# Kernel tuning notes

Measured on AMD Instinct MI355X. Metric: run time of the kernel, lower is better.

The kernel has to match this reference:

```python
import jax, jax.numpy as jnp
import numpy as np

B, D, N = 2048, 512, 100000


def setup_inputs() -> dict:
    key = jax.random.key(0)
    k1, k2, k3 = jax.random.split(key, 3)
    queries = jax.random.normal(k1, (B, D), dtype=jnp.float32)
    X = jax.random.normal(k2, (N, D), dtype=jnp.float32)
    Y = jax.random.randint(k3, (N,), 0, 2, dtype=jnp.int64)
    return {"queries": queries, "X": X, "Y": Y, "K": 5}


def reference(queries, X, Y, K):
    # Pairwise squared Euclidean distance: ||q||^2 - 2 q.X^T + ||x||^2.
    # Use negative distance so lax.top_k returns nearest neighbors.
    q2 = jnp.sum(queries * queries, axis=1, keepdims=True)        # [B, 1]
    x2 = jnp.sum(X * X, axis=1)                                   # [N]
    neg_dist = 2.0 * (queries @ X.T) - q2 - x2[None, :]           # [B, N]
    _, idx = jax.lax.top_k(neg_dist, K)                           # [B, K]
    # Gather neighbor labels and count votes (fraction of class-1 neighbors).
    neighbor_labels = Y[idx].astype(jnp.float32)                  # [B, K]
    votes = jnp.mean(neighbor_labels, axis=1)                     # [B]
    # tf.pad(tf.expand_dims(votes, 1), [[0,0],[0,1]]) -> [B, 2]
    return jnp.pad(votes[:, None], ((0, 0), (0, 1)))
```

## Files before the change

### kernel.cpp

```cpp
#include <hip/hip_runtime.h>
#include <math.h>

typedef unsigned int   u32;
typedef unsigned short u16;
typedef short short8 __attribute__((ext_vector_type(8)));
typedef float f32x4  __attribute__((ext_vector_type(4)));

constexpr int B    = 2048;
constexpr int D    = 512;
constexpr int N    = 100000;
constexpr int KTOP = 5;
constexpr int NK   = 16;

constexpr int NPART    = 64;
constexpr int CHUNK    = 1568;
constexpr int PGPART   = CHUNK / 16;
constexpr int NPTS_PAD = NPART * CHUNK;
constexpr int NPG      = NPTS_PAD / 16;
constexpr int ITERS    = PGPART;

__device__ __forceinline__ u16 f2bf(float f) {
    u32 u = __float_as_uint(f);
    return (u16)((u + 0x7fffu + ((u >> 16) & 1u)) >> 16);
}

__device__ __forceinline__ void gld_lds16(const void* g, void* l) {
    __builtin_amdgcn_global_load_lds((const __attribute__((address_space(1))) u32*)g,
                                     (__attribute__((address_space(3))) u32*)l, 16, 0, 0);
}

__device__ __forceinline__ void ins5(float (&s)[KTOP], int (&x)[KTOP], float v, int p) {
    if (v > s[KTOP - 1]) {
        s[KTOP - 1] = v; x[KTOP - 1] = p;
#pragma unroll
        for (int k = KTOP - 1; k > 0; --k) {
            if (s[k] > s[k - 1]) {
                float tf = s[k]; s[k] = s[k - 1]; s[k - 1] = tf;
                int   tg = x[k]; x[k] = x[k - 1]; x[k - 1] = tg;
            }
        }
    }
}

__device__ __forceinline__ void merge_xor(float (&s)[KTOP], int (&x)[KTOP], int mask) {
    float bs[KTOP], as[KTOP]; int bx[KTOP], ax[KTOP];
#pragma unroll
    for (int k = 0; k < KTOP; ++k) {
        bs[k] = __shfl_xor(s[k], mask); bx[k] = __shfl_xor(x[k], mask);
        as[k] = s[k]; ax[k] = x[k];
    }
#pragma unroll
    for (int k = 0; k < KTOP; ++k) {
        bool ta = (as[0] > bs[0]) || ((as[0] == bs[0]) && (ax[0] < bx[0]));
        s[k] = ta ? as[0] : bs[0];
        x[k] = ta ? ax[0] : bx[0];
#pragma unroll
        for (int m = 0; m < KTOP - 1; ++m) {
            as[m] = ta ? as[m + 1] : as[m];     ax[m] = ta ? ax[m + 1] : ax[m];
            bs[m] = ta ? bs[m]     : bs[m + 1]; bx[m] = ta ? bx[m]     : bx[m + 1];
        }
        as[KTOP - 1] = ta ? -INFINITY : as[KTOP - 1];
        bs[KTOP - 1] = ta ? bs[KTOP - 1] : -INFINITY;
    }
}

__global__ void prep_q(const float* __restrict__ Q, u16* __restrict__ Qbf) {
    int tid  = blockIdx.x * 256 + threadIdx.x;
    int q    = tid >> 6;
    int koct = tid & 63;
    const float4* src = (const float4*)(Q + (size_t)q * D + koct * 8);
    float4 a = src[0], b = src[1];
    u32 p0 = (u32)f2bf(a.x) | ((u32)f2bf(a.y) << 16);
    u32 p1 = (u32)f2bf(a.z) | ((u32)f2bf(a.w) << 16);
    u32 p2 = (u32)f2bf(b.x) | ((u32)f2bf(b.y) << 16);
    u32 p3 = (u32)f2bf(b.z) | ((u32)f2bf(b.w) << 16);
    int frag = (q >> 4) * NK + (koct >> 2);
    int lane = (q & 15) + 16 * (koct & 3);
    *(uint4*)(Qbf + (size_t)frag * 512 + lane * 8) = make_uint4(p0, p1, p2, p3);
}

__global__ void prep_x2(const float* __restrict__ X, u16* __restrict__ Xbf,
                        float* __restrict__ x2) {
    __shared__ float psum[4][16];
    const int t = threadIdx.x, lane = t & 63, wave = t >> 6;
    const int pg    = blockIdx.x;
    const int point = pg * 16 + (lane & 15);
    float ssum = 0.f;
#pragma unroll
    for (int u = 0; u < 4; ++u) {
        int k0i = wave * 4 + u;
        int k   = k0i * 32 + ((lane >> 4) << 3);
        uint4 o = make_uint4(0u, 0u, 0u, 0u);
        if (point < N) {
            const float4* src = (const float4*)(X + (size_t)point * D + k);
            float4 a = src[0], b = src[1];
            ssum = fmaf(a.x, a.x, ssum); ssum = fmaf(a.y, a.y, ssum);
            ssum = fmaf(a.z, a.z, ssum); ssum = fmaf(a.w, a.w, ssum);
            ssum = fmaf(b.x, b.x, ssum); ssum = fmaf(b.y, b.y, ssum);
            ssum = fmaf(b.z, b.z, ssum); ssum = fmaf(b.w, b.w, ssum);
            o.x = (u32)f2bf(a.x) | ((u32)f2bf(a.y) << 16);
            o.y = (u32)f2bf(a.z) | ((u32)f2bf(a.w) << 16);
            o.z = (u32)f2bf(b.x) | ((u32)f2bf(b.y) << 16);
            o.w = (u32)f2bf(b.z) | ((u32)f2bf(b.w) << 16);
        }
        *(uint4*)(Xbf + ((size_t)pg * 16 + k0i) * 512 + lane * 8) = o;
    }
    ssum += __shfl_xor(ssum, 16);
    ssum += __shfl_xor(ssum, 32);
    if (lane < 16) psum[wave][lane] = ssum;
    __syncthreads();
    if (t < 16) {
        float s = psum[0][t] + psum[1][t] + psum[2][t] + psum[3][t];
        x2[pg * 16 + t] = (pg * 16 + t < N) ? s : INFINITY;
    }
}

__global__ void x2_kernel(const float* __restrict__ X, float* __restrict__ x2, int total) {
    int lane = threadIdx.x & 63;
    int wid  = (int)((blockIdx.x * blockDim.x + threadIdx.x) >> 6);
    if (wid >= total) return;
    if (wid >= N) { if (lane == 0) x2[wid] = INFINITY; return; }
    const float* row = X + (size_t)wid * D;
    float s = 0.f;
    for (int c = lane; c < D; c += 64) { float v = row[c]; s = fmaf(v, v, s); }
#pragma unroll
    for (int off = 32; off > 0; off >>= 1) s += __shfl_down(s, off);
    if (lane == 0) x2[wid] = s;
}

__launch_bounds__(256, 4)
__global__ void knn_qreg(const u16* __restrict__ Xbf, const u16* __restrict__ Qbf,
                         const float* __restrict__ x2g,
                         float* __restrict__ cand_s, int* __restrict__ cand_i) {
    __shared__ __attribute__((aligned(16))) u16 Afr[2][16 * 512];
    const int t    = threadIdx.x;
    const int lane = t & 63;
    const int wave = t >> 6;
    const int quad = lane >> 4;
    const int col  = lane & 15;
    const int part = blockIdx.x;
    const int qb   = blockIdx.y;
    const int pg0    = part * PGPART;
    const int pstart = part * CHUNK;

    const int qg = qb * 4 + wave;
    short8 bq[16];
#pragma unroll
    for (int k0i = 0; k0i < 16; ++k0i)
        bq[k0i] = *(const short8*)(Qbf + ((size_t)qg * 16 + k0i) * 512 + lane * 8);
    asm volatile("" ::: "memory");

    float ss[KTOP]; int si[KTOP];
#pragma unroll
    for (int k = 0; k < KTOP; ++k) { ss[k] = -INFINITY; si[k] = 0x7fffffff; }

    auto issue = [&](int it, int bsel) {
        const size_t pgA = (size_t)(pg0 + it);
        const u16* src = Xbf + (pgA * 16 + wave * 4) * 512 + (lane << 3);
        u16* dst = Afr[bsel] + (wave * 4) * 512;
#pragma unroll
        for (int f = 0; f < 4; ++f)
            gld_lds16(src + f * 512, dst + f * 512);
    };

    issue(0, 0);
    for (int it = 0; it < ITERS; ++it) {
        const int bsel = it & 1;
        __syncthreads();
        if (it + 1 < ITERS) issue(it + 1, bsel ^ 1);
        const int PA = pstart + it * 16;
        float4 xx = *(const float4*)(x2g + PA + quad * 4);

        f32x4 acc = (f32x4)0.f;
#pragma unroll
        for (int k0i = 0; k0i < 16; ++k0i) {
            short8 af = *(const short8*)&Afr[bsel][k0i * 512 + lane * 8];
            acc = __builtin_amdgcn_mfma_f32_16x16x32_bf16(af, bq[k0i], acc, 0, 0, 0);
        }
        const int gbase = PA + quad * 4;
        float s0 = fmaf(2.f, acc[0], -xx.x);
        float s1 = fmaf(2.f, acc[1], -xx.y);
        float s2 = fmaf(2.f, acc[2], -xx.z);
        float s3 = fmaf(2.f, acc[3], -xx.w);
        float mx = fmaxf(fmaxf(s0, s1), fmaxf(s2, s3));
        if (mx > ss[KTOP - 1]) {
            ins5(ss, si, s0, gbase + 0); ins5(ss, si, s1, gbase + 1);
            ins5(ss, si, s2, gbase + 2); ins5(ss, si, s3, gbase + 3);
        }
    }

    merge_xor(ss, si, 16); merge_xor(ss, si, 32);
    if (quad == 0) {
        int q = qg * 16 + col;
        size_t base = ((size_t)q * NPART + part) * KTOP;
#pragma unroll
        for (int k = 0; k < KTOP; ++k) { cand_s[base + k] = ss[k]; cand_i[base + k] = si[k]; }
    }
}

__launch_bounds__(256)
__global__ void knn_conv(const float* __restrict__ X, const u16* __restrict__ Qbf,
                         const float* __restrict__ x2g,
                         float* __restrict__ cand_s, int* __restrict__ cand_i) {
    __shared__ __attribute__((aligned(16))) u16 Bfr[16 * 512];
    __shared__ __attribute__((aligned(16))) u16 Afr[4 * 512];
    __shared__ float x2s[64];
    const int t = threadIdx.x, lane = t & 63, wave = t >> 6;
    const int quad = lane >> 4, col = lane & 15;
    const int qb = blockIdx.x, part = blockIdx.y;
    const int pstart = part * 782;
    const int pend   = min(pstart + 782, N);

    float ss[4][KTOP]; int si[4][KTOP];
#pragma unroll
    for (int j = 0; j < 4; ++j)
#pragma unroll
        for (int k = 0; k < KTOP; ++k) { ss[j][k] = -INFINITY; si[j][k] = 0x7fffffff; }

    const int nsub = (pend - pstart + 63) / 64;
    for (int sbi = 0; sbi < nsub; ++sbi) {
        const int sb = pstart + sbi * 64;
        __syncthreads();
        if (t < 64) x2s[t] = (sb + t < pend) ? x2g[sb + t] : INFINITY;
        f32x4 acc[4][4];
#pragma unroll
        for (int i = 0; i < 4; ++i)
#pragma unroll
            for (int j = 0; j < 4; ++j) acc[i][j] = (f32x4)0.f;
        for (int k0i = 0; k0i < NK; ++k0i) {
            const int k0 = k0i * 32;
            __syncthreads();
            {
                int prow = sb + wave * 16 + col;
                if (prow >= pend) prow = pend - 1;
                const float4* src = (const float4*)(X + (size_t)prow * D + k0 + quad * 8);
                float4 a = src[0], b = src[1];
                u32 p0 = (u32)f2bf(a.x) | ((u32)f2bf(a.y) << 16);
                u32 p1 = (u32)f2bf(a.z) | ((u32)f2bf(a.w) << 16);
                u32 p2 = (u32)f2bf(b.x) | ((u32)f2bf(b.y) << 16);
                u32 p3 = (u32)f2bf(b.z) | ((u32)f2bf(b.w) << 16);
                *(uint4*)(Afr + wave * 512 + lane * 8) = make_uint4(p0, p1, p2, p3);
            }
#pragma unroll
            for (int j = 0; j < 4; ++j) {
                int qgrp = qb * 16 + wave * 4 + j;
                gld_lds16(Qbf + ((size_t)qgrp * NK + k0i) * 512 + lane * 8,
                          (void*)(Bfr + (wave * 4 + j) * 512));
            }
            __syncthreads();
            short8 af[4], bqf[4];
#pragma unroll
            for (int i = 0; i < 4; ++i) af[i] = *(const short8*)(Afr + i * 512 + lane * 8);
#pragma unroll
            for (int j = 0; j < 4; ++j) bqf[j] = *(const short8*)(Bfr + (wave * 4 + j) * 512 + lane * 8);
#pragma unroll
            for (int i = 0; i < 4; ++i)
#pragma unroll
                for (int j = 0; j < 4; ++j)
                    acc[i][j] = __builtin_amdgcn_mfma_f32_16x16x32_bf16(af[i], bqf[j], acc[i][j], 0, 0, 0);
        }
#pragma unroll
        for (int i = 0; i < 4; ++i) {
            int pb = 16 * i + quad * 4;
#pragma unroll
            for (int j = 0; j < 4; ++j)
#pragma unroll
                for (int r = 0; r < 4; ++r)
                    ins5(ss[j], si[j], 2.f * acc[i][j][r] - x2s[pb + r], sb + pb + r);
        }
    }
#pragma unroll
    for (int j = 0; j < 4; ++j) { merge_xor(ss[j], si[j], 16); merge_xor(ss[j], si[j], 32); }
    if (quad == 0) {
#pragma unroll
        for (int j = 0; j < 4; ++j) {
            int qg = qb * 256 + wave * 64 + j * 16 + col;
            size_t base = ((size_t)qg * 128 + part) * KTOP;
#pragma unroll
            for (int k = 0; k < KTOP; ++k) { cand_s[base + k] = ss[j][k]; cand_i[base + k] = si[j][k]; }
        }
    }
}

__launch_bounds__(256)
__global__ void finalize(const float* __restrict__ Q, const float* __restrict__ X,
                         const float* __restrict__ x2g, const int* __restrict__ Y,
                         const float* __restrict__ cand_s, const int* __restrict__ cand_i,
                         float* __restrict__ out, int npart) {
    __shared__ float scs[4][96];
    __shared__ int   sis[4][96];
    const int t = threadIdx.x, lane = t & 63, w = t >> 6;
    const int q = blockIdx.x * 4 + w;
    const int perlane = npart * KTOP / 16;

    if (lane < 16) {
        float ls[KTOP]; int li[KTOP];
#pragma unroll
        for (int k = 0; k < KTOP; ++k) { ls[k] = -INFINITY; li[k] = 0x7fffffff; }
        const float* cs = cand_s + (size_t)q * npart * KTOP + lane * perlane;
        const int*   ci = cand_i + (size_t)q * npart * KTOP + lane * perlane;
        for (int c = 0; c < perlane; ++c) {
            float s = cs[c]; int p = ci[c];
            if (s > ls[KTOP - 1] || (s == ls[KTOP - 1] && p < li[KTOP - 1])) {
                ls[KTOP - 1] = s; li[KTOP - 1] = p;
#pragma unroll
                for (int k = KTOP - 1; k > 0; --k) {
                    bool up = (ls[k] > ls[k - 1]) || (ls[k] == ls[k - 1] && li[k] < li[k - 1]);
                    if (up) {
                        float tf = ls[k]; ls[k] = ls[k - 1]; ls[k - 1] = tf;
                        int   tg = li[k]; li[k] = li[k - 1]; li[k - 1] = tg;
                    }
                }
            }
        }
#pragma unroll
        for (int k = 0; k < KTOP; ++k) { scs[w][lane * KTOP + k] = ls[k]; sis[w][lane * KTOP + k] = li[k]; }
    }
    __syncthreads();
    if (lane == 0) {
        float bs[16]; int bx[16];
#pragma unroll
        for (int m = 0; m < 16; ++m) { bs[m] = -INFINITY; bx[m] = 0x7fffffff; }
        for (int c = 0; c < 80; ++c) {
            float s = scs[w][c]; int p = sis[w][c];
            if (s > bs[15] || (s == bs[15] && p < bx[15])) {
                bs[15] = s; bx[15] = p;
#pragma unroll
                for (int m = 15; m > 0; --m) {
                    bool up = (bs[m] > bs[m - 1]) || (bs[m] == bs[m - 1] && bx[m] < bx[m - 1]);
                    if (up) {
                        float tf = bs[m]; bs[m] = bs[m - 1]; bs[m - 1] = tf;
                        int   tg = bx[m]; bx[m] = bx[m - 1]; bx[m - 1] = tg;
                    }
                }
            }
        }
#pragma unroll
        for (int m = 0; m < 16; ++m) sis[w][80 + m] = bx[m];
    }
    __syncthreads();
    const int c = lane & 15, seg = lane >> 4;
    int idx = sis[w][80 + c];
    const float4* xr = (const float4*)(X + (size_t)idx * D);
    const float4* qr = (const float4*)(Q + (size_t)q * D);
    float d = 0.f;
    for (int u = seg * 32; u < seg * 32 + 32; ++u) {
        float4 a = qr[u], b = xr[u];
        d = fmaf(a.x, b.x, d); d = fmaf(a.y, b.y, d);
        d = fmaf(a.z, b.z, d); d = fmaf(a.w, b.w, d);
    }
    d += __shfl_xor(d, 16);
    d += __shfl_xor(d, 32);
    float sc = 2.f * d - x2g[idx];
    if (seg == 0) scs[w][80 + c] = sc;
    __syncthreads();
    if (lane == 0) {
        float bs[KTOP]; int bx[KTOP];
#pragma unroll
        for (int k = 0; k < KTOP; ++k) { bs[k] = -INFINITY; bx[k] = 0x7fffffff; }
        for (int c2 = 0; c2 < 16; ++c2) {
            float s = scs[w][80 + c2]; int p = sis[w][80 + c2];
            if (s > bs[KTOP - 1] || (s == bs[KTOP - 1] && p < bx[KTOP - 1])) {
                bs[KTOP - 1] = s; bx[KTOP - 1] = p;
#pragma unroll
                for (int k = KTOP - 1; k > 0; --k) {
                    bool up = (bs[k] > bs[k - 1]) || (bs[k] == bs[k - 1] && bx[k] < bx[k - 1]);
                    if (up) {
                        float tf = bs[k]; bs[k] = bs[k - 1]; bs[k - 1] = tf;
                        int   tg = bx[k]; bx[k] = bx[k - 1]; bx[k - 1] = tg;
                    }
                }
            }
        }
        float sum = 0.f;
#pragma unroll
        for (int k = 0; k < KTOP; ++k) sum += (float)Y[bx[k]];
        out[2 * q]     = sum * 0.2f;
        out[2 * q + 1] = 0.f;
    }
}

extern "C" void kernel_launch(void* const* d_in, const int* in_sizes, int n_in,
                              void* d_out, int out_size, void* d_ws, size_t ws_size,
                              hipStream_t stream) {
    const float* Qf = (const float*)d_in[0];
    const float* Xf = (const float*)d_in[1];
    const int*   Y  = (const int*)d_in[2];
    float* out = (float*)d_out;
    char* ws = (char*)d_ws;

    constexpr size_t XBF_B  = (size_t)NPG * NK * 1024;
    constexpr size_t QBF_B  = 2097152;
    constexpr size_t X2_B   = (size_t)NPTS_PAD * 4;
    constexpr size_t CAND_B = (size_t)B * NPART * KTOP * 4;
    constexpr size_t NEED   = XBF_B + QBF_B + X2_B + 2 * CAND_B;

    if (ws_size >= NEED) {
        u16*   Xbf    = (u16*)ws;
        u16*   Qbf    = (u16*)(ws + XBF_B);
        float* x2     = (float*)(ws + XBF_B + QBF_B);
        float* cand_s = (float*)(ws + XBF_B + QBF_B + X2_B);
        int*   cand_i = (int*)  (ws + XBF_B + QBF_B + X2_B + CAND_B);
        hipLaunchKernelGGL(prep_q,   dim3(512),       dim3(256), 0, stream, Qf, Qbf);
        hipLaunchKernelGGL(prep_x2,  dim3(NPG),       dim3(256), 0, stream, Xf, Xbf, x2);
        hipLaunchKernelGGL(knn_qreg, dim3(NPART, 32), dim3(256), 0, stream, Xbf, Qbf, x2, cand_s, cand_i);
        hipLaunchKernelGGL(finalize, dim3(B / 4),     dim3(256), 0, stream, Qf, Xf, x2, Y, cand_s, cand_i, out, NPART);
    } else {
        u16*   Qbf    = (u16*)ws;
        float* x2     = (float*)(ws + 2097152);
        float* cand_s = (float*)(ws + 2497152);
        int*   cand_i = (int*)  (ws + 7740032);
        hipLaunchKernelGGL(prep_q,    dim3(512),      dim3(256), 0, stream, Qf, Qbf);
        hipLaunchKernelGGL(x2_kernel, dim3(N / 4),    dim3(256), 0, stream, Xf, x2, N);
        hipLaunchKernelGGL(knn_conv,  dim3(8, 128),   dim3(256), 0, stream, Xf, Qbf, x2, cand_s, cand_i);
        hipLaunchKernelGGL(finalize,  dim3(B / 4),    dim3(256), 0, stream, Qf, Xf, x2, Y, cand_s, cand_i, out, 128);
    }
}
```

Baseline: 660.2 us.

## Switch KNN distance tiles to 32x32x16 MFMA with 32-point, 32-query fragments

Moves the main distance kernel from 16x16x32 to 32x32x16 bf16 MFMA. Each wave now handles 32 queries and 32 points per iteration, and the query fragments held in registers grow to 32 vectors. The X and Q bf16 prep layouts change to match. Partitions go from 64 to 48 and the LDS double buffer is split into two K-halves, which adds a second barrier per iteration. Larger tiles should improve MFMA throughput and halve the X reloads per query, at the cost of more registers (occupancy hint lowered to 3) and more insertion work per step.

```diff
diff --git a/kernel.cpp b/kernel.cpp
--- a/kernel.cpp
+++ b/kernel.cpp
@@ -4,7 +4,8 @@
 typedef unsigned int   u32;
 typedef unsigned short u16;
 typedef short short8 __attribute__((ext_vector_type(8)));
-typedef float f32x4  __attribute__((ext_vector_type(4)));
+typedef float f32x4   __attribute__((ext_vector_type(4)));
+typedef float f32x16  __attribute__((ext_vector_type(16)));
 
 constexpr int B    = 2048;
 constexpr int D    = 512;
@@ -12,12 +13,11 @@
 constexpr int KTOP = 5;
 constexpr int NK   = 16;
 
-constexpr int NPART    = 64;
-constexpr int CHUNK    = 1568;
-constexpr int PGPART   = CHUNK / 16;
+constexpr int NPART    = 48;
+constexpr int CHUNK    = 2112;
+constexpr int ITERS    = CHUNK / 32;
 constexpr int NPTS_PAD = NPART * CHUNK;
-constexpr int NPG      = NPTS_PAD / 16;
-constexpr int ITERS    = PGPART;
+constexpr int NPG32    = NPTS_PAD / 32;
 
 __device__ __forceinline__ u16 f2bf(float f) {
     u32 u = __float_as_uint(f);
@@ -64,7 +64,23 @@
     }
 }
 
-__global__ void prep_q(const float* __restrict__ Q, u16* __restrict__ Qbf) {
+__global__ void prep_q32(const float* __restrict__ Q, u16* __restrict__ Qbf) {
+    int tid  = blockIdx.x * 256 + threadIdx.x;
+    int q    = tid >> 6;
+    int koct = tid & 63;
+    const float4* src = (const float4*)(Q + (size_t)q * D + koct * 8);
+    float4 a = src[0], b = src[1];
+    u32 p0 = (u32)f2bf(a.x) | ((u32)f2bf(a.y) << 16);
+    u32 p1 = (u32)f2bf(a.z) | ((u32)f2bf(a.w) << 16);
+    u32 p2 = (u32)f2bf(b.x) | ((u32)f2bf(b.y) << 16);
+    u32 p3 = (u32)f2bf(b.z) | ((u32)f2bf(b.w) << 16);
+    int kstep = koct >> 1, octet = koct & 1;
+    int lane  = (q & 31) + 32 * octet;
+    size_t frag = (size_t)(q >> 5) * 32 + kstep;
+    *(uint4*)(Qbf + (frag * 64 + lane) * 8) = make_uint4(p0, p1, p2, p3);
+}
+
+__global__ void prep_q16(const float* __restrict__ Q, u16* __restrict__ Qbf) {
     int tid  = blockIdx.x * 256 + threadIdx.x;
     int q    = tid >> 6;
     int koct = tid & 63;
@@ -81,15 +97,16 @@
 
 __global__ void prep_x2(const float* __restrict__ X, u16* __restrict__ Xbf,
                         float* __restrict__ x2) {
-    __shared__ float psum[4][16];
+    __shared__ float psum[4][32];
     const int t = threadIdx.x, lane = t & 63, wave = t >> 6;
     const int pg    = blockIdx.x;
-    const int point = pg * 16 + (lane & 15);
+    const int pt    = lane & 31, octet = lane >> 5;
+    const int point = pg * 32 + pt;
     float ssum = 0.f;
 #pragma unroll
-    for (int u = 0; u < 4; ++u) {
-        int k0i = wave * 4 + u;
-        int k   = k0i * 32 + ((lane >> 4) << 3);
+    for (int u = 0; u < 8; ++u) {
+        int kstep = wave * 8 + u;
+        int k     = kstep * 16 + octet * 8;
         uint4 o = make_uint4(0u, 0u, 0u, 0u);
         if (point < N) {
             const float4* src = (const float4*)(X + (size_t)point * D + k);
@@ -103,15 +120,14 @@
             o.z = (u32)f2bf(b.x) | ((u32)f2bf(b.y) << 16);
             o.w = (u32)f2bf(b.z) | ((u32)f2bf(b.w) << 16);
         }
-        *(uint4*)(Xbf + ((size_t)pg * 16 + k0i) * 512 + lane * 8) = o;
-    }
-    ssum += __shfl_xor(ssum, 16);
+        *(uint4*)(Xbf + (((size_t)pg * 32 + kstep) * 64 + lane) * 8) = o;
+    }
     ssum += __shfl_xor(ssum, 32);
-    if (lane < 16) psum[wave][lane] = ssum;
+    if (octet == 0) psum[wave][pt] = ssum;
     __syncthreads();
-    if (t < 16) {
+    if (t < 32) {
         float s = psum[0][t] + psum[1][t] + psum[2][t] + psum[3][t];
-        x2[pg * 16 + t] = (pg * 16 + t < N) ? s : INFINITY;
+        x2[pg * 32 + t] = (pg * 32 + t < N) ? s : INFINITY;
     }
 }
 
@@ -128,7 +144,7 @@
     if (lane == 0) x2[wid] = s;
 }
 
-__launch_bounds__(256, 4)
+__launch_bounds__(256, 3)
 __global__ void knn_qreg(const u16* __restrict__ Xbf, const u16* __restrict__ Qbf,
                          const float* __restrict__ x2g,
                          float* __restrict__ cand_s, int* __restrict__ cand_i) {
@@ -136,62 +152,83 @@
     const int t    = threadIdx.x;
     const int lane = t & 63;
     const int wave = t >> 6;
-    const int quad = lane >> 4;
-    const int col  = lane & 15;
+    const int hid  = lane >> 5;
+    const int col  = lane & 31;
     const int part = blockIdx.x;
     const int qb   = blockIdx.y;
-    const int pg0    = part * PGPART;
+    const int pg0    = part * ITERS;
     const int pstart = part * CHUNK;
 
     const int qg = qb * 4 + wave;
-    short8 bq[16];
-#pragma unroll
-    for (int k0i = 0; k0i < 16; ++k0i)
-        bq[k0i] = *(const short8*)(Qbf + ((size_t)qg * 16 + k0i) * 512 + lane * 8);
+    short8 bq[32];
+#pragma unroll
+    for (int ks = 0; ks < 32; ++ks)
+        bq[ks] = *(const short8*)(Qbf + (((size_t)qg * 32 + ks) * 64 + lane) * 8);
     asm volatile("" ::: "memory");
 
     float ss[KTOP]; int si[KTOP];
 #pragma unroll
     for (int k = 0; k < KTOP; ++k) { ss[k] = -INFINITY; si[k] = 0x7fffffff; }
 
-    auto issue = [&](int it, int bsel) {
-        const size_t pgA = (size_t)(pg0 + it);
-        const u16* src = Xbf + (pgA * 16 + wave * 4) * 512 + (lane << 3);
-        u16* dst = Afr[bsel] + (wave * 4) * 512;
+    auto issue = [&](int it, int h) {
+        const size_t fb = ((size_t)(pg0 + it) * 32 + h * 16 + wave * 4) * 64;
+        const u16* src = Xbf + (fb + lane) * 8;
+        u16* dst = Afr[h] + ((wave * 4) * 64 + lane) * 8;
 #pragma unroll
         for (int f = 0; f < 4; ++f)
-            gld_lds16(src + f * 512, dst + f * 512);
+            gld_lds16(src + (size_t)f * 512, dst + f * 512);
     };
 
     issue(0, 0);
     for (int it = 0; it < ITERS; ++it) {
-        const int bsel = it & 1;
         __syncthreads();
-        if (it + 1 < ITERS) issue(it + 1, bsel ^ 1);
-        const int PA = pstart + it * 16;
-        float4 xx = *(const float4*)(x2g + PA + quad * 4);
-
-        f32x4 acc = (f32x4)0.f;
-#pragma unroll
-        for (int k0i = 0; k0i < 16; ++k0i) {
-            short8 af = *(const short8*)&Afr[bsel][k0i * 512 + lane * 8];
-            acc = __builtin_amdgcn_mfma_f32_16x16x32_bf16(af, bq[k0i], acc, 0, 0, 0);
-        }
-        const int gbase = PA + quad * 4;
-        float s0 = fmaf(2.f, acc[0], -xx.x);
-        float s1 = fmaf(2.f, acc[1], -xx.y);
-        float s2 = fmaf(2.f, acc[2], -xx.z);
-        float s3 = fmaf(2.f, acc[3], -xx.w);
-        float mx = fmaxf(fmaxf(s0, s1), fmaxf(s2, s3));
+        issue(it, 1);
+        f32x16 acc = (f32x16)0.f;
+#pragma unroll
+        for (int k = 0; k < 16; ++k) {
+            short8 af = *(const short8*)&Afr[0][k * 512 + lane * 8];
+            acc = __builtin_amdgcn_mfma_f32_32x32x16_bf16(af, bq[k], acc, 0, 0, 0);
+        }
+        __syncthreads();
+        if (it + 1 < ITERS) issue(it + 1, 0);
+#pragma unroll
+        for (int k = 0; k < 16; ++k) {
+            short8 af = *(const short8*)&Afr[1][k * 512 + lane * 8];
+            acc = __builtin_amdgcn_mfma_f32_32x32x16_bf16(af, bq[16 + k], acc, 0, 0, 0);
+        }
+        const int PA = pstart + it * 32 + hid * 4;
+        float4 xx0 = *(const float4*)(x2g + PA);
+        float4 xx1 = *(const float4*)(x2g + PA + 8);
+        float4 xx2 = *(const float4*)(x2g + PA + 16);
+        float4 xx3 = *(const float4*)(x2g + PA + 24);
+        float s0  = fmaf(2.f, acc[0],  -xx0.x), s1  = fmaf(2.f, acc[1],  -xx0.y);
+        float s2  = fmaf(2.f, acc[2],  -xx0.z), s3  = fmaf(2.f, acc[3],  -xx0.w);
+        float s4  = fmaf(2.f, acc[4],  -xx1.x), s5  = fmaf(2.f, acc[5],  -xx1.y);
+        float s6  = fmaf(2.f, acc[6],  -xx1.z), s7  = fmaf(2.f, acc[7],  -xx1.w);
+        float s8  = fmaf(2.f, acc[8],  -xx2.x), s9  = fmaf(2.f, acc[9],  -xx2.y);
+        float s10 = fmaf(2.f, acc[10], -xx2.z), s11 = fmaf(2.f, acc[11], -xx2.w);
+        float s12 = fmaf(2.f, acc[12], -xx3.x), s13 = fmaf(2.f, acc[13], -xx3.y);
+        float s14 = fmaf(2.f, acc[14], -xx3.z), s15 = fmaf(2.f, acc[15], -xx3.w);
+        float m0 = fmaxf(fmaxf(s0, s1),   fmaxf(s2, s3));
+        float m1 = fmaxf(fmaxf(s4, s5),   fmaxf(s6, s7));
+        float m2 = fmaxf(fmaxf(s8, s9),   fmaxf(s10, s11));
+        float m3 = fmaxf(fmaxf(s12, s13), fmaxf(s14, s15));
+        float mx = fmaxf(fmaxf(m0, m1), fmaxf(m2, m3));
         if (mx > ss[KTOP - 1]) {
-            ins5(ss, si, s0, gbase + 0); ins5(ss, si, s1, gbase + 1);
-            ins5(ss, si, s2, gbase + 2); ins5(ss, si, s3, gbase + 3);
-        }
-    }
-
-    merge_xor(ss, si, 16); merge_xor(ss, si, 32);
-    if (quad == 0) {
-        int q = qg * 16 + col;
+            ins5(ss, si, s0,  PA + 0);  ins5(ss, si, s1,  PA + 1);
+            ins5(ss, si, s2,  PA + 2);  ins5(ss, si, s3,  PA + 3);
+            ins5(ss, si, s4,  PA + 8);  ins5(ss, si, s5,  PA + 9);
+            ins5(ss, si, s6,  PA + 10); ins5(ss, si, s7,  PA + 11);
+            ins5(ss, si, s8,  PA + 16); ins5(ss, si, s9,  PA + 17);
+            ins5(ss, si, s10, PA + 18); ins5(ss, si, s11, PA + 19);
+            ins5(ss, si, s12, PA + 24); ins5(ss, si, s13, PA + 25);
+            ins5(ss, si, s14, PA + 26); ins5(ss, si, s15, PA + 27);
+        }
+    }
+
+    merge_xor(ss, si, 32);
+    if (hid == 0) {
+        int q = qg * 32 + col;
         size_t base = ((size_t)q * NPART + part) * KTOP;
 #pragma unroll
         for (int k = 0; k < KTOP; ++k) { cand_s[base + k] = ss[k]; cand_i[base + k] = si[k]; }
@@ -389,7 +426,7 @@
     float* out = (float*)d_out;
     char* ws = (char*)d_ws;
 
-    constexpr size_t XBF_B  = (size_t)NPG * NK * 1024;
+    constexpr size_t XBF_B  = (size_t)NPTS_PAD * D * 2;
     constexpr size_t QBF_B  = 2097152;
     constexpr size_t X2_B   = (size_t)NPTS_PAD * 4;
     constexpr size_t CAND_B = (size_t)B * NPART * KTOP * 4;
@@ -401,16 +438,16 @@
         float* x2     = (float*)(ws + XBF_B + QBF_B);
         float* cand_s = (float*)(ws + XBF_B + QBF_B + X2_B);
         int*   cand_i = (int*)  (ws + XBF_B + QBF_B + X2_B + CAND_B);
-        hipLaunchKernelGGL(prep_q,   dim3(512),       dim3(256), 0, stream, Qf, Qbf);
-        hipLaunchKernelGGL(prep_x2,  dim3(NPG),       dim3(256), 0, stream, Xf, Xbf, x2);
-        hipLaunchKernelGGL(knn_qreg, dim3(NPART, 32), dim3(256), 0, stream, Xbf, Qbf, x2, cand_s, cand_i);
+        hipLaunchKernelGGL(prep_q32, dim3(512),       dim3(256), 0, stream, Qf, Qbf);
+        hipLaunchKernelGGL(prep_x2,  dim3(NPG32),     dim3(256), 0, stream, Xf, Xbf, x2);
+        hipLaunchKernelGGL(knn_qreg, dim3(NPART, 16), dim3(256), 0, stream, Xbf, Qbf, x2, cand_s, cand_i);
         hipLaunchKernelGGL(finalize, dim3(B / 4),     dim3(256), 0, stream, Qf, Xf, x2, Y, cand_s, cand_i, out, NPART);
     } else {
         u16*   Qbf    = (u16*)ws;
         float* x2     = (float*)(ws + 2097152);
         float* cand_s = (float*)(ws + 2497152);
         int*   cand_i = (int*)  (ws + 7740032);
-        hipLaunchKernelGGL(prep_q,    dim3(512),      dim3(256), 0, stream, Qf, Qbf);
+        hipLaunchKernelGGL(prep_q16,  dim3(512),      dim3(256), 0, stream, Qf, Qbf);
         hipLaunchKernelGGL(x2_kernel, dim3(N / 4),    dim3(256), 0, stream, Xf, x2, N);
         hipLaunchKernelGGL(knn_conv,  dim3(8, 128),   dim3(256), 0, stream, Xf, Qbf, x2, cand_s, cand_i);
         hipLaunchKernelGGL(finalize,  dim3(B / 4),    dim3(256), 0, stream, Qf, Xf, x2, Y, cand_s, cand_i, out, 128);
```

Measured after the change: 687.4 us. 1.04x slower.
